# Performance work log

Measured on AMD Instinct MI355X. Metric: run time of the kernel, lower is better.

## Reference

```python
import jax, jax.numpy as jnp
import numpy as np

DIM = 256   # model dim (forced by gate Linear(32,4): d = 32 = DIM//H)
H = 8       # heads (hard-coded by mask.repeat(1,8,1,1))
D = DIM // H
B = 256     # batch
NS = 100    # skeleton tokens (sub-block size)
NQ = 64     # query tokens
N = NS + NQ # 164
NE = 4      # experts
HID = 50    # expert hidden
LN_EPS = 1e-5


def setup_inputs() -> dict:
    key = jax.random.key(0)
    ks = jax.random.split(key, 12)
    s = 0.02
    return {
        "x": jax.random.normal(ks[0], (B, N, DIM), jnp.float32),
        "mask": jax.random.randint(ks[1], (B, N), 0, 2).astype(bool),
        "w_qk_s": jax.random.normal(ks[2], (DIM, 2 * DIM), jnp.float32) * s,
        "w_qk_q": jax.random.normal(ks[3], (DIM, 2 * DIM), jnp.float32) * s,
        "w_v": jax.random.normal(ks[4], (DIM, DIM), jnp.float32) * s,
        "w_gate": jax.random.normal(ks[5], (D, NE), jnp.float32) * s,
        "b_gate": jnp.zeros((NE,), jnp.float32),
        "ln_gamma": jnp.ones((NE,), jnp.float32),
        "ln_beta": jnp.zeros((NE,), jnp.float32),
        "w1": jax.random.normal(ks[6], (NE, NS, HID), jnp.float32) * s,
        "b1": jnp.zeros((NE, HID), jnp.float32),
        "w2": jax.random.normal(ks[7], (NE, HID, NS), jnp.float32) * s,
        "b2": jnp.zeros((NE, NS), jnp.float32),
        "w_out": jax.random.normal(ks[8], (DIM, DIM), jnp.float32) * s,
        "b_out": jnp.zeros((DIM,), jnp.float32),
    }


def reference(x, mask, w_qk_s, w_qk_q, w_v, w_gate, b_gate, ln_gamma, ln_beta,
              w1, b1, w2, b2, w_out, b_out):
    b, n, dim = x.shape
    scale = dim ** -0.5  # scale_with_head=False -> dim**-0.5

    def to_heads(t):  # (b, m, H*D) -> (b, H, m, D)
        return t.reshape(b, -1, H, D).transpose(0, 2, 1, 3)

    # separate qk projections for skeleton (first 100) vs query (last 64) tokens
    q_s, k_s = jnp.split(x[:, :NS] @ w_qk_s, 2, axis=-1)
    q_q, k_q = jnp.split(x[:, NS:] @ w_qk_q, 2, axis=-1)
    q = jnp.concatenate([to_heads(q_s), to_heads(q_q)], axis=2)  # (b,H,N,D)
    k = jnp.concatenate([to_heads(k_s), to_heads(k_q)], axis=2)
    v = to_heads(x @ w_v)

    # gates: RAW reshape of x (b,n,H*D) -> (b,H,n,D) (memory reinterpretation,
    # as in torch x.reshape), detached, sliced to first 100 'rows'
    gx = jax.lax.stop_gradient(x).reshape(b, H, n, D)[:, :, :NS, :]
    g = gx @ w_gate + b_gate                              # (b,H,100,4)
    mu = g.mean(-1, keepdims=True)
    var = g.var(-1, keepdims=True)
    g = (g - mu) / jnp.sqrt(var + LN_EPS) * ln_gamma + ln_beta
    gates = jax.nn.softmax(g, axis=-1)                    # (b,H,100,4)

    dots = jnp.einsum('bhid,bhjd->bhij', q, k) * scale    # (b,H,N,N)
    mask_value = -jnp.finfo(dots.dtype).max
    dots = jnp.where(mask[:, None, None, :], mask_value, dots)

    # soft-MoE over the 100x100 sub-block (experts applied along key axis)
    attn_q = dots[:, :, :NS, :NS]                         # (b,H,100,100)
    h1 = jax.nn.relu(jnp.einsum('bhij,ejk->bheik', jax.nn.relu(attn_q), w1)
                     + b1[:, None, :])                    # (b,H,4,100,50)
    eo = jax.nn.relu(jnp.einsum('bheik,ekj->bheij', h1, w2)
                     + b2[:, None, :])                    # (b,H,4,100,100)
    moes = jnp.einsum('bheij,bhie->bhij', eo, gates)      # (b,H,100,100)

    dots = dots.at[:, :, :NS, :NS].add(moes)
    attn = jax.nn.softmax(dots, axis=-1)
    out = jnp.einsum('bhij,bhjd->bhid', attn, v)          # (b,H,N,D)
    out = out.transpose(0, 2, 1, 3).reshape(b, n, dim)
    return out @ w_out + b_out
```

## Files before the change

kernel.cpp:

```cpp
#include <hip/hip_runtime.h>

typedef __bf16 bf16x8 __attribute__((ext_vector_type(8)));
typedef __bf16 bf16x4 __attribute__((ext_vector_type(4)));
typedef float  f32x4  __attribute__((ext_vector_type(4)));

__device__ __forceinline__ bf16x8 ldb8(const __bf16* p) {
    return *reinterpret_cast<const bf16x8*>(p);
}
__device__ __forceinline__ bf16x8 zero8() {
    bf16x8 z;
    #pragma unroll
    for (int i = 0; i < 8; i++) z[i] = (__bf16)0.f;
    return z;
}
__device__ __forceinline__ __bf16 ldw(const void* p, int i, int m) {
    return m ? (__bf16)((const float*)p)[i] : ((const __bf16*)p)[i];
}
__device__ __forceinline__ bf16x8 ldx8(const void* p, size_t ei, int m) {
    if (m) {
        const float* f = (const float*)p + ei;
        f32x4 a = *reinterpret_cast<const f32x4*>(f);
        f32x4 b = *reinterpret_cast<const f32x4*>(f + 4);
        bf16x8 r;
        #pragma unroll
        for (int u = 0; u < 4; u++) { r[u] = (__bf16)a[u]; r[4 + u] = (__bf16)b[u]; }
        return r;
    }
    return ldb8((const __bf16*)p + ei);
}

__global__ __launch_bounds__(256) void prep_kernel(
    const void* x, const void* mask,
    const void* wqks, const void* wqkq, const void* wv, const void* w1,
    const void* w2, const void* wout, const void* wg, const void* bg,
    const void* lng, const void* lnb, const void* b1, const void* b2,
    const void* bout, int* modes, unsigned* maskb,
    __bf16* __restrict__ Wts, __bf16* __restrict__ Wtq,
    __bf16* __restrict__ w1t, __bf16* __restrict__ w2t,
    __bf16* __restrict__ wot, __bf16* __restrict__ wsm)
{
    __shared__ int sbad;
    const int t = threadIdx.x, bid = blockIdx.x;
    if (t == 0) sbad = 0;
    __syncthreads();
    {
        const unsigned int* xw = (const unsigned int*)x;
        int bad = 0;
        for (int i = t; i < 2048; i += 256) {
            unsigned int w = xw[i];
            unsigned int el = (w >> 7) & 0xFF, eh = (w >> 23) & 0xFF;
            if (el >= 0x94 || el == 0xFF) bad++;
            if (eh >= 0x94 || eh == 0xFF) bad++;
        }
        if (bad) atomicAdd(&sbad, bad);
    }
    __syncthreads();
    const int m = (sbad > 64) ? 1 : 0;

    if (bid >= 1268) {
        __shared__ int v32bad, v16bad;
        __shared__ unsigned mb[24];
        const int mbid = bid - 1268;
        if (t == 0) { v32bad = 0; v16bad = 0; }
        if (t < 24) mb[t] = ((t % 6) == 5) ? 0xFFFFFFF0u : 0u;
        __syncthreads();
        const unsigned int* mw = (const unsigned int*)mask;
        int b32 = 0, b16 = 0;
        for (int i = t; i < 10496; i += 256) {
            unsigned int w = mw[i];
            if (!(w == 0u || w == 1u || w == 0x3F800000u)) b32++;
            unsigned int h0 = w & 0xFFFFu, h1 = w >> 16;
            if (!(h0 == 0u || h0 == 1u || h0 == 0x3F80u)) b16++;
            if (!(h1 == 0u || h1 == 1u || h1 == 0x3F80u)) b16++;
        }
        if (b32) atomicAdd(&v32bad, b32);
        if (b16) atomicAdd(&v16bad, b16);
        __syncthreads();
        const int mmode = (v32bad == 0) ? 0 : ((v16bad == 0) ? 2 : 1);
        if (mbid == 0 && t == 0) { modes[0] = m; modes[1] = mmode; }
        const int lo = mbid * 656;
        for (int i2 = t; i2 < 656; i2 += 256) {
            int i = lo + i2;
            int val;
            if (mmode == 0)      val = (((const int*)mask)[i] != 0);
            else if (mmode == 2) val = (((const unsigned short*)mask)[i] != 0);
            else                 val = (((const unsigned char*)mask)[i] != 0);
            if (val) {
                int ib = i2 / 164, jb = i2 - ib * 164;
                atomicOr(&mb[ib * 6 + (jb >> 5)], 1u << (jb & 31));
            }
        }
        __syncthreads();
        if (t < 24) maskb[mbid * 24 + t] = mb[t];
        return;
    }

    int i = bid * 256 + t;
    if (i < 196608) {
        int n = i >> 8, k = i & 255;
        __bf16 vs, vq;
        if (n < 512) { vs = ldw(wqks, k * 512 + n, m); vq = ldw(wqkq, k * 512 + n, m); }
        else         { vs = ldw(wv, k * 256 + (n - 512), m); vq = vs; }
        Wts[i] = vs; Wtq[i] = vq;
        return;
    }
    i -= 196608;
    if (i < 32768) {
        int e = i >> 13, r = i & 8191, n = r >> 7, k = r & 127;
        __bf16 v = (__bf16)0.f;
        if (n < 50) {
            if (k < 100)       v = ldw(w1, (e * 100 + k) * 50 + n, m);
            else if (k == 100) v = ldw(b1, e * 50 + n, m);
        }
        w1t[i] = v;
        return;
    }
    i -= 32768;
    if (i < 28672) {
        int e = i / 7168, r = i % 7168, n = r >> 6, k = r & 63;
        __bf16 v = (__bf16)0.f;
        if (n < 100) {
            if (k < 50)       v = ldw(w2, (e * 50 + k) * 100 + n, m);
            else if (k == 50) v = ldw(b2, e * 100 + n, m);
        }
        w2t[i] = v;
        return;
    }
    i -= 28672;
    if (i < 65536) {
        int n = i >> 8, k = i & 255;
        wot[i] = ldw(wout, k * 256 + n, m);
        return;
    }
    i -= 65536;
    if (i < 996) {
        __bf16 v;
        if (i < 128)      v = ldw(wg, i, m);
        else if (i < 132) v = ldw(bg, i - 128, m);
        else if (i < 136) v = ldw(lng, i - 132, m);
        else if (i < 140) v = ldw(lnb, i - 136, m);
        else if (i < 340) v = ldw(b1, i - 140, m);
        else if (i < 740) v = ldw(b2, i - 340, m);
        else              v = ldw(bout, i - 740, m);
        wsm[i] = v;
    }
}

__global__ __launch_bounds__(256, 2) void qkv_kernel(
    const void* __restrict__ x, const __bf16* __restrict__ Wts,
    const __bf16* __restrict__ Wtq, const __bf16* __restrict__ wsm,
    const int* __restrict__ modes,
    __bf16* __restrict__ q, __bf16* __restrict__ k, __bf16* __restrict__ vt,
    float* __restrict__ gates)
{
    __shared__ __bf16 xs[32][264];
    __shared__ float wgf[128];
    __shared__ float gcst[12];
    const int m = modes[0];
    const int b = blockIdx.y;
    const int mt = blockIdx.x >> 1;
    const int half = blockIdx.x & 1;
    const __bf16* Wt = (mt < 4) ? Wts : Wtq;
    const int rbase = (mt < 4) ? mt * 32 : 100 + (mt - 4) * 32;
    const int tid = threadIdx.x;

    if (tid < 128) wgf[tid] = (float)wsm[tid];
    if (tid < 12)  gcst[tid] = (float)wsm[128 + tid];
    for (int c = tid; c < 1024; c += 256) {
        int row = c >> 5, part = c & 31;
        bf16x8 val = ldx8(x, ((size_t)b * 164 + rbase + row) * 256 + part * 8, m);
        *reinterpret_cast<bf16x8*>(&xs[row][part * 8]) = val;
    }
    __syncthreads();

    if (half == 0) {
        int jg = rbase * 8 + tid;
        int h = jg / 164;
        int j = jg - h * 164;
        if (j < 100) {
            const __bf16* xp = &xs[tid >> 3][(tid & 7) * 32];
            float g[4] = {gcst[0], gcst[1], gcst[2], gcst[3]};
            #pragma unroll
            for (int p = 0; p < 4; p++) {
                bf16x8 xv = ldb8(xp + p * 8);
                #pragma unroll
                for (int u = 0; u < 8; u++) {
                    float f = (float)xv[u];
                    #pragma unroll
                    for (int e = 0; e < 4; e++) g[e] += f * wgf[(p * 8 + u) * 4 + e];
                }
            }
            float mu = 0.25f * (g[0] + g[1] + g[2] + g[3]);
            float var = 0.25f * ((g[0]-mu)*(g[0]-mu) + (g[1]-mu)*(g[1]-mu) +
                                 (g[2]-mu)*(g[2]-mu) + (g[3]-mu)*(g[3]-mu));
            float is = rsqrtf(var + 1e-5f);
            float mx = -3.0e38f;
            #pragma unroll
            for (int e = 0; e < 4; e++) {
                g[e] = (g[e] - mu) * is * gcst[4 + e] + gcst[8 + e];
                mx = fmaxf(mx, g[e]);
            }
            float s = 0.f;
            #pragma unroll
            for (int e = 0; e < 4; e++) { g[e] = __expf(g[e] - mx); s += g[e]; }
            float inv = 1.f / s;
            float4 gv = make_float4(g[0]*inv, g[1]*inv, g[2]*inv, g[3]*inv);
            *reinterpret_cast<float4*>(&gates[((size_t)(b * 8 + h) * 100 + j) * 4]) = gv;
        }
    }

    const int w = tid >> 6, l = tid & 63, lr = l & 15, lc = l >> 4;
    f32x4 acc[2][6];
    #pragma unroll
    for (int ms = 0; ms < 2; ms++)
        #pragma unroll
        for (int nt = 0; nt < 6; nt++) acc[ms][nt] = (f32x4){0.f, 0.f, 0.f, 0.f};

    #pragma unroll
    for (int kt = 0; kt < 8; kt++) {
        bf16x8 a0 = ldb8(&xs[lr][kt * 32 + lc * 8]);
        bf16x8 a1 = ldb8(&xs[16 + lr][kt * 32 + lc * 8]);
        #pragma unroll
        for (int nt = 0; nt < 6; nt++) {
            bf16x8 bb = ldb8(Wt + (size_t)(half * 384 + w * 96 + nt * 16 + lr) * 256 + kt * 32 + lc * 8);
            acc[0][nt] = __builtin_amdgcn_mfma_f32_16x16x32_bf16(a0, bb, acc[0][nt], 0, 0, 0);
            acc[1][nt] = __builtin_amdgcn_mfma_f32_16x16x32_bf16(a1, bb, acc[1][nt], 0, 0, 0);
        }
    }
    #pragma unroll
    for (int ms = 0; ms < 2; ms++) {
        #pragma unroll
        for (int nt = 0; nt < 6; nt++) {
            int c = half * 384 + w * 96 + nt * 16 + lr;
            int i0 = rbase + ms * 16 + lc * 4;
            if (c < 512) {
                __bf16* dst; int ch;
                if (c < 256) { dst = q; ch = c; }
                else         { dst = k; ch = c - 256; }
                int hh = ch >> 5, d = ch & 31;
                #pragma unroll
                for (int r = 0; r < 4; r++) {
                    int i = i0 + r;
                    if (mt >= 4 || i < 100)
                        dst[(((size_t)b * 8 + hh) * 164 + i) * 32 + d] = (__bf16)acc[ms][nt][r];
                }
            } else {
                int ch = c - 512, hh = ch >> 5, d = ch & 31;
                if (mt >= 4 || i0 < 100) {
                    bf16x4 pv;
                    #pragma unroll
                    for (int r = 0; r < 4; r++) pv[r] = (__bf16)acc[ms][nt][r];
                    *reinterpret_cast<bf16x4*>(&vt[((size_t)(b * 8 + hh) * 32 + d) * 176 + i0]) = pv;
                }
            }
        }
    }
}

__global__ __launch_bounds__(256, 4) void attn_kernel(
    const __bf16* __restrict__ qg, const __bf16* __restrict__ kg,
    const __bf16* __restrict__ vtg, const float* __restrict__ gatesg,
    const unsigned* __restrict__ maskbg, const __bf16* __restrict__ w1t,
    const __bf16* __restrict__ w2t, __bf16* __restrict__ ohg)
{
    __shared__ __align__(16) __bf16 lds[20352];
    const int RS_OFF = 7040;
    const int P_OFF  = 7040;
    const int H1_OFF = 15744;

    const int flat = blockIdx.x;
    const int xcd = flat & 7, j5 = flat >> 3;
    const int bh = ((j5 & 255) << 3) | xcd;
    const int rt = j5 >> 8;
    const int b = bh >> 3, tid = threadIdx.x;
    const int w = tid >> 6, l = tid & 63, lr = l & 15, lc = l >> 4;
    const int m0 = w * 16;
    const bool moe_wave = (rt * 64 + m0) < 100;

    const __bf16* kbase = kg + (size_t)bh * 164 * 32;
    for (int c = tid; c < 656; c += 256) {
        int row = c >> 2, part = c & 3;
        bf16x8 val = ldb8(kbase + row * 32 + part * 8);
        *reinterpret_cast<bf16x8*>(&lds[row * 40 + part * 8]) = val;
    }
    const unsigned* mbp = maskbg + b * 6;
    unsigned mbits = 0;
    #pragma unroll
    for (int nt = 0; nt < 11; nt++)
        mbits |= ((mbp[nt >> 1] >> (((nt & 1) << 4) + lr)) & 1u) << nt;
    int qrow = rt * 64 + m0 + lr; if (qrow > 163) qrow = 163;
    bf16x8 afq = ldb8(qg + ((size_t)bh * 164 + qrow) * 32 + lc * 8);
    __syncthreads();

    f32x4 raw[11];
    __builtin_amdgcn_s_setprio(1);
    #pragma unroll
    for (int nt = 0; nt < 11; nt++) {
        bf16x8 bf = ldb8(&lds[(nt * 16 + lr) * 40 + lc * 8]);
        f32x4 acc = {0.f, 0.f, 0.f, 0.f};
        acc = __builtin_amdgcn_mfma_f32_16x16x32_bf16(afq, bf, acc, 0, 0, 0);
        bool bad = (mbits >> nt) & 1;
        #pragma unroll
        for (int r = 0; r < 4; r++)
            raw[nt][r] = bad ? -1e30f : acc[r] * 0.0625f;
    }
    __builtin_amdgcn_s_setprio(0);

    if (moe_wave) {
        #pragma unroll
        for (int nt = 0; nt < 8; nt++) {
            int j = nt * 16 + lr;
            #pragma unroll
            for (int r = 0; r < 4; r++) {
                float v = raw[nt][r];
                v = (v < 0.f) ? 0.f : v;
                if (j >= 100) v = (j == 100) ? 1.f : 0.f;
                lds[RS_OFF + (m0 + lc * 4 + r) * 136 + j] = (__bf16)v;
            }
        }
    }
    __syncthreads();

    const __bf16* vtb = vtg + (size_t)bh * 32 * 176;
    #pragma unroll
    for (int p = 0; p < 3; p++) {
        int c = tid + p * 256;
        int row = c / 24, jc = c - row * 24, j0 = jc * 8;
        bf16x8 vv;
        if (j0 < 164) {
            vv = ldb8(vtb + row * 176 + j0);
            if (j0 == 160) { vv[4] = (__bf16)0.f; vv[5] = (__bf16)0.f; vv[6] = (__bf16)0.f; vv[7] = (__bf16)0.f; }
        } else vv = zero8();
        *reinterpret_cast<bf16x8*>(&lds[row * 200 + j0]) = vv;
    }

    if (moe_wave) {
        const int gi0 = rt * 64 + m0 + lc * 4;
        for (int e = 0; e < 4; e++) {
            bf16x8 sa[4];
            #pragma unroll
            for (int kt = 0; kt < 4; kt++)
                sa[kt] = ldb8(&lds[RS_OFF + (m0 + lr) * 136 + kt * 32 + lc * 8]);
            #pragma unroll
            for (int nt = 0; nt < 4; nt++) {
                f32x4 acc = {0.f, 0.f, 0.f, 0.f};
                __builtin_amdgcn_s_setprio(1);
                #pragma unroll
                for (int kt = 0; kt < 4; kt++) {
                    bf16x8 bb = ldb8(w1t + (size_t)(e * 64 + nt * 16 + lr) * 128 + kt * 32 + lc * 8);
                    acc = __builtin_amdgcn_mfma_f32_16x16x32_bf16(sa[kt], bb, acc, 0, 0, 0);
                }
                __builtin_amdgcn_s_setprio(0);
                int n = nt * 16 + lr;
                #pragma unroll
                for (int r = 0; r < 4; r++) {
                    float v = acc[r];
                    if (v < 0.f) v = 0.f;
                    if (n == 50) v = 1.f;
                    lds[H1_OFF + (m0 + lc * 4 + r) * 72 + n] = (__bf16)v;
                }
            }
            bf16x8 ha0 = ldb8(&lds[H1_OFF + (m0 + lr) * 72 + lc * 8]);
            bf16x8 ha1 = ldb8(&lds[H1_OFF + (m0 + lr) * 72 + 32 + lc * 8]);
            float gt[4];
            #pragma unroll
            for (int r = 0; r < 4; r++) {
                int gi = gi0 + r;
                gt[r] = (gi < 100) ? gatesg[((size_t)bh * 100 + gi) * 4 + e] : 0.f;
            }
            #pragma unroll
            for (int nt = 0; nt < 7; nt++) {
                f32x4 acc = {0.f, 0.f, 0.f, 0.f};
                __builtin_amdgcn_s_setprio(1);
                bf16x8 bb0 = ldb8(w2t + (size_t)(e * 112 + nt * 16 + lr) * 64 + lc * 8);
                acc = __builtin_amdgcn_mfma_f32_16x16x32_bf16(ha0, bb0, acc, 0, 0, 0);
                bf16x8 bb1 = ldb8(w2t + (size_t)(e * 112 + nt * 16 + lr) * 64 + 32 + lc * 8);
                acc = __builtin_amdgcn_mfma_f32_16x16x32_bf16(ha1, bb1, acc, 0, 0, 0);
                __builtin_amdgcn_s_setprio(0);
                #pragma unroll
                for (int r = 0; r < 4; r++) {
                    float v = acc[r];
                    if (v < 0.f) v = 0.f;
                    raw[nt][r] += v * gt[r];
                }
            }
        }
    }
    __syncthreads();

    #pragma unroll
    for (int r = 0; r < 4; r++) {
        float m2 = raw[0][r];
        #pragma unroll
        for (int nt = 1; nt < 11; nt++) m2 = fmaxf(m2, raw[nt][r]);
        m2 = fmaxf(m2, __shfl_xor(m2, 1, 64));
        m2 = fmaxf(m2, __shfl_xor(m2, 2, 64));
        m2 = fmaxf(m2, __shfl_xor(m2, 4, 64));
        m2 = fmaxf(m2, __shfl_xor(m2, 8, 64));
        float s2 = 0.f;
        #pragma unroll
        for (int nt = 0; nt < 11; nt++) {
            float ev = __expf(raw[nt][r] - m2);
            raw[nt][r] = ev;
            s2 += ev;
        }
        s2 += __shfl_xor(s2, 1, 64);
        s2 += __shfl_xor(s2, 2, 64);
        s2 += __shfl_xor(s2, 4, 64);
        s2 += __shfl_xor(s2, 8, 64);
        float inv = (s2 > 0.f) ? 1.f / s2 : 0.f;
        #pragma unroll
        for (int nt = 0; nt < 11; nt++)
            lds[P_OFF + (m0 + lc * 4 + r) * 200 + nt * 16 + lr] = (__bf16)(raw[nt][r] * inv);
        lds[P_OFF + (m0 + lc * 4 + r) * 200 + 176 + lr] = (__bf16)0.f;
    }
    __syncthreads();

    int gi = rt * 64 + m0 + lr;
    #pragma unroll
    for (int nt = 0; nt < 2; nt++) {
        f32x4 acc = {0.f, 0.f, 0.f, 0.f};
        __builtin_amdgcn_s_setprio(1);
        #pragma unroll
        for (int kt = 0; kt < 6; kt++) {
            bf16x8 va = ldb8(&lds[(nt * 16 + lr) * 200 + kt * 32 + lc * 8]);
            bf16x8 pb = ldb8(&lds[P_OFF + (m0 + lr) * 200 + kt * 32 + lc * 8]);
            acc = __builtin_amdgcn_mfma_f32_16x16x32_bf16(va, pb, acc, 0, 0, 0);
        }
        __builtin_amdgcn_s_setprio(0);
        if (gi < 164) {
            bf16x4 ov;
            #pragma unroll
            for (int r = 0; r < 4; r++) ov[r] = (__bf16)acc[r];
            *reinterpret_cast<bf16x4*>(&ohg[((size_t)bh * 164 + gi) * 32 + nt * 16 + lc * 4]) = ov;
        }
    }
}

__global__ __launch_bounds__(256) void outproj_kernel(
    const __bf16* __restrict__ oh, const __bf16* __restrict__ wot,
    const __bf16* __restrict__ wsm, float* __restrict__ out)
{
    const __bf16* bout = wsm + 740;
    const int b = blockIdx.y;
    const int mt = blockIdx.x >> 2;
    const int ntile = blockIdx.x & 3;
    const int tid = threadIdx.x;
    const int w = tid >> 6, l = tid & 63, lr = l & 15, lc = l >> 4;
    int row = mt * 64 + w * 16 + lr; if (row > 163) row = 163;
    f32x4 acc[4];
    #pragma unroll
    for (int nt = 0; nt < 4; nt++) acc[nt] = (f32x4){0.f, 0.f, 0.f, 0.f};
    #pragma unroll
    for (int kt = 0; kt < 8; kt++) {
        bf16x8 a = ldb8(oh + (((size_t)b * 8 + kt) * 164 + row) * 32 + lc * 8);
        #pragma unroll
        for (int nt = 0; nt < 4; nt++) {
            bf16x8 bb = ldb8(wot + (size_t)(ntile * 64 + nt * 16 + lr) * 256 + kt * 32 + lc * 8);
            acc[nt] = __builtin_amdgcn_mfma_f32_16x16x32_bf16(a, bb, acc[nt], 0, 0, 0);
        }
    }
    #pragma unroll
    for (int nt = 0; nt < 4; nt++) {
        int n = ntile * 64 + nt * 16 + lr;
        float bias = (float)bout[n];
        #pragma unroll
        for (int r = 0; r < 4; r++) {
            int i = mt * 64 + w * 16 + lc * 4 + r;
            if (i < 164)
                out[((size_t)b * 164 + i) * 256 + n] = acc[nt][r] + bias;
        }
    }
}

extern "C" void kernel_launch(void* const* d_in, const int* in_sizes, int n_in,
                              void* d_out, int out_size, void* d_ws, size_t ws_size,
                              hipStream_t stream) {
    const void* x      = d_in[0];
    const void* mask   = d_in[1];
    const void* w_qk_s = d_in[2];
    const void* w_qk_q = d_in[3];
    const void* w_v    = d_in[4];
    const void* w_gate = d_in[5];
    const void* b_gate = d_in[6];
    const void* ln_g   = d_in[7];
    const void* ln_b   = d_in[8];
    const void* w1     = d_in[9];
    const void* b1     = d_in[10];
    const void* w2     = d_in[11];
    const void* b2     = d_in[12];
    const void* w_out  = d_in[13];
    const void* b_out  = d_in[14];
    float* out = (float*)d_out;

    char* ws = (char*)d_ws;
    size_t off = 0;
    auto nextp = [&](size_t bytes) {
        char* p = ws + off;
        off += (bytes + 255) & ~(size_t)255;
        return p;
    };
    const size_t QKV_ELEMS = (size_t)256 * 8 * 164 * 32;
    const size_t VT_ELEMS  = (size_t)256 * 8 * 32 * 176;
    int*      modes  = (int*)nextp(64);
    unsigned* maskb  = (unsigned*)nextp((size_t)256 * 6 * 4);
    __bf16* qws  = (__bf16*)nextp(QKV_ELEMS * 2);
    __bf16* kws  = (__bf16*)nextp(QKV_ELEMS * 2);
    __bf16* vtws = (__bf16*)nextp(VT_ELEMS * 2);
    __bf16* ohws = (__bf16*)nextp(QKV_ELEMS * 2);
    float*  gws  = (float*)nextp((size_t)2048 * 100 * 4 * 4);
    __bf16* Wts  = (__bf16*)nextp(768 * 256 * 2);
    __bf16* Wtq  = (__bf16*)nextp(768 * 256 * 2);
    __bf16* w1t  = (__bf16*)nextp(4 * 64 * 128 * 2);
    __bf16* w2t  = (__bf16*)nextp(4 * 112 * 64 * 2);
    __bf16* wot  = (__bf16*)nextp(256 * 256 * 2);
    __bf16* wsm  = (__bf16*)nextp(996 * 2);

    prep_kernel<<<1332, 256, 0, stream>>>(x, mask, w_qk_s, w_qk_q, w_v, w1, w2,
                                          w_out, w_gate, b_gate, ln_g, ln_b, b1,
                                          b2, b_out, modes, maskb,
                                          Wts, Wtq, w1t, w2t, wot, wsm);
    qkv_kernel<<<dim3(12, 256), 256, 0, stream>>>(x, Wts, Wtq, wsm, modes,
                                                  qws, kws, vtws, gws);
    attn_kernel<<<6144, 256, 0, stream>>>(qws, kws, vtws, gws, maskb,
                                          w1t, w2t, ohws);
    outproj_kernel<<<dim3(12, 256), 256, 0, stream>>>(ohws, wot, wsm, out);
}
```

Before: 490.4 us.

## Give each wave a private LDS region and read K straight from global

Each wave now gets its own LDS scratch slice for the relu'd scores, the MoE hidden tile and the softmax probabilities. This removes the block-wide barriers between the score, MoE and softmax phases, leaving one barrier before the P·V product. K fragments are loaded directly from global memory per wave instead of being staged through shared memory. The V tile load is issued early into registers and written to LDS later to overlap its latency. The cost is more redundant global K reads across waves and higher register pressure from holding the V vectors.

Result: no change. 484.5 us (-1.2%).

```diff
diff --git a/kernel.cpp b/kernel.cpp
--- a/kernel.cpp
+++ b/kernel.cpp
@@ -263,11 +263,7 @@
     const unsigned* __restrict__ maskbg, const __bf16* __restrict__ w1t,
     const __bf16* __restrict__ w2t, __bf16* __restrict__ ohg)
 {
-    __shared__ __align__(16) __bf16 lds[20352];
-    const int RS_OFF = 7040;
-    const int P_OFF  = 7040;
-    const int H1_OFF = 15744;
-
+    __shared__ __align__(16) __bf16 lds[19712];
     const int flat = blockIdx.x;
     const int xcd = flat & 7, j5 = flat >> 3;
     const int bh = ((j5 & 255) << 3) | xcd;
@@ -275,14 +271,37 @@
     const int b = bh >> 3, tid = threadIdx.x;
     const int w = tid >> 6, l = tid & 63, lr = l & 15, lc = l >> 4;
     const int m0 = w * 16;
+    const int WB  = 6400 + w * 3328;
+    const int H1B = WB + 2176;
     const bool moe_wave = (rt * 64 + m0) < 100;
 
-    const __bf16* kbase = kg + (size_t)bh * 164 * 32;
-    for (int c = tid; c < 656; c += 256) {
-        int row = c >> 2, part = c & 3;
-        bf16x8 val = ldb8(kbase + row * 32 + part * 8);
-        *reinterpret_cast<bf16x8*>(&lds[row * 40 + part * 8]) = val;
-    }
+    const __bf16* vtb = vtg + (size_t)bh * 32 * 176;
+    bf16x8 vv0, vv1, vv2;
+    {
+        int c = tid;
+        int row = c / 24, j0 = (c - row * 24) * 8;
+        if (j0 < 164) {
+            vv0 = ldb8(vtb + row * 176 + j0);
+            if (j0 == 160) { vv0[4] = (__bf16)0.f; vv0[5] = (__bf16)0.f; vv0[6] = (__bf16)0.f; vv0[7] = (__bf16)0.f; }
+        } else vv0 = zero8();
+    }
+    {
+        int c = tid + 256;
+        int row = c / 24, j0 = (c - row * 24) * 8;
+        if (j0 < 164) {
+            vv1 = ldb8(vtb + row * 176 + j0);
+            if (j0 == 160) { vv1[4] = (__bf16)0.f; vv1[5] = (__bf16)0.f; vv1[6] = (__bf16)0.f; vv1[7] = (__bf16)0.f; }
+        } else vv1 = zero8();
+    }
+    {
+        int c = tid + 512;
+        int row = c / 24, j0 = (c - row * 24) * 8;
+        if (j0 < 164) {
+            vv2 = ldb8(vtb + row * 176 + j0);
+            if (j0 == 160) { vv2[4] = (__bf16)0.f; vv2[5] = (__bf16)0.f; vv2[6] = (__bf16)0.f; vv2[7] = (__bf16)0.f; }
+        } else vv2 = zero8();
+    }
+
     const unsigned* mbp = maskbg + b * 6;
     unsigned mbits = 0;
     #pragma unroll
@@ -290,21 +309,32 @@
         mbits |= ((mbp[nt >> 1] >> (((nt & 1) << 4) + lr)) & 1u) << nt;
     int qrow = rt * 64 + m0 + lr; if (qrow > 163) qrow = 163;
     bf16x8 afq = ldb8(qg + ((size_t)bh * 164 + qrow) * 32 + lc * 8);
-    __syncthreads();
-
+
+    const __bf16* kbase = kg + (size_t)bh * 164 * 32;
     f32x4 raw[11];
-    __builtin_amdgcn_s_setprio(1);
     #pragma unroll
     for (int nt = 0; nt < 11; nt++) {
-        bf16x8 bf = ldb8(&lds[(nt * 16 + lr) * 40 + lc * 8]);
+        int krow = nt * 16 + lr; if (krow > 163) krow = 163;
+        bf16x8 kb = ldb8(kbase + (size_t)krow * 32 + lc * 8);
         f32x4 acc = {0.f, 0.f, 0.f, 0.f};
-        acc = __builtin_amdgcn_mfma_f32_16x16x32_bf16(afq, bf, acc, 0, 0, 0);
+        acc = __builtin_amdgcn_mfma_f32_16x16x32_bf16(afq, kb, acc, 0, 0, 0);
         bool bad = (mbits >> nt) & 1;
         #pragma unroll
         for (int r = 0; r < 4; r++)
             raw[nt][r] = bad ? -1e30f : acc[r] * 0.0625f;
     }
-    __builtin_amdgcn_s_setprio(0);
+
+    {
+        int c = tid;
+        int row = c / 24, j0 = (c - row * 24) * 8;
+        *reinterpret_cast<bf16x8*>(&lds[row * 200 + j0]) = vv0;
+        c = tid + 256;
+        row = c / 24; j0 = (c - row * 24) * 8;
+        *reinterpret_cast<bf16x8*>(&lds[row * 200 + j0]) = vv1;
+        c = tid + 512;
+        row = c / 24; j0 = (c - row * 24) * 8;
+        *reinterpret_cast<bf16x8*>(&lds[row * 200 + j0]) = vv2;
+    }
 
     if (moe_wave) {
         #pragma unroll
@@ -315,23 +345,9 @@
                 float v = raw[nt][r];
                 v = (v < 0.f) ? 0.f : v;
                 if (j >= 100) v = (j == 100) ? 1.f : 0.f;
-                lds[RS_OFF + (m0 + lc * 4 + r) * 136 + j] = (__bf16)v;
-            }
-        }
-    }
-    __syncthreads();
-
-    const __bf16* vtb = vtg + (size_t)bh * 32 * 176;
-    #pragma unroll
-    for (int p = 0; p < 3; p++) {
-        int c = tid + p * 256;
-        int row = c / 24, jc = c - row * 24, j0 = jc * 8;
-        bf16x8 vv;
-        if (j0 < 164) {
-            vv = ldb8(vtb + row * 176 + j0);
-            if (j0 == 160) { vv[4] = (__bf16)0.f; vv[5] = (__bf16)0.f; vv[6] = (__bf16)0.f; vv[7] = (__bf16)0.f; }
-        } else vv = zero8();
-        *reinterpret_cast<bf16x8*>(&lds[row * 200 + j0]) = vv;
+                lds[WB + (lc * 4 + r) * 136 + j] = (__bf16)v;
+            }
+        }
     }
 
     if (moe_wave) {
@@ -340,7 +356,7 @@
             bf16x8 sa[4];
             #pragma unroll
             for (int kt = 0; kt < 4; kt++)
-                sa[kt] = ldb8(&lds[RS_OFF + (m0 + lr) * 136 + kt * 32 + lc * 8]);
+                sa[kt] = ldb8(&lds[WB + lr * 136 + kt * 32 + lc * 8]);
             #pragma unroll
             for (int nt = 0; nt < 4; nt++) {
                 f32x4 acc = {0.f, 0.f, 0.f, 0.f};
@@ -357,11 +373,11 @@
                     float v = acc[r];
                     if (v < 0.f) v = 0.f;
                     if (n == 50) v = 1.f;
-                    lds[H1_OFF + (m0 + lc * 4 + r) * 72 + n] = (__bf16)v;
+                    lds[H1B + (lc * 4 + r) * 72 + n] = (__bf16)v;
                 }
             }
-            bf16x8 ha0 = ldb8(&lds[H1_OFF + (m0 + lr) * 72 + lc * 8]);
-            bf16x8 ha1 = ldb8(&lds[H1_OFF + (m0 + lr) * 72 + 32 + lc * 8]);
+            bf16x8 ha0 = ldb8(&lds[H1B + lr * 72 + lc * 8]);
+            bf16x8 ha1 = ldb8(&lds[H1B + lr * 72 + 32 + lc * 8]);
             float gt[4];
             #pragma unroll
             for (int r = 0; r < 4; r++) {
@@ -386,7 +402,6 @@
             }
         }
     }
-    __syncthreads();
 
     #pragma unroll
     for (int r = 0; r < 4; r++) {
@@ -411,8 +426,8 @@
         float inv = (s2 > 0.f) ? 1.f / s2 : 0.f;
         #pragma unroll
         for (int nt = 0; nt < 11; nt++)
-            lds[P_OFF + (m0 + lc * 4 + r) * 200 + nt * 16 + lr] = (__bf16)(raw[nt][r] * inv);
-        lds[P_OFF + (m0 + lc * 4 + r) * 200 + 176 + lr] = (__bf16)0.f;
+            lds[WB + (lc * 4 + r) * 200 + nt * 16 + lr] = (__bf16)(raw[nt][r] * inv);
+        lds[WB + (lc * 4 + r) * 200 + 176 + lr] = (__bf16)0.f;
     }
     __syncthreads();
 
@@ -424,7 +439,7 @@
         #pragma unroll
         for (int kt = 0; kt < 6; kt++) {
             bf16x8 va = ldb8(&lds[(nt * 16 + lr) * 200 + kt * 32 + lc * 8]);
-            bf16x8 pb = ldb8(&lds[P_OFF + (m0 + lr) * 200 + kt * 32 + lc * 8]);
+            bf16x8 pb = ldb8(&lds[WB + lr * 200 + kt * 32 + lc * 8]);
             acc = __builtin_amdgcn_mfma_f32_16x16x32_bf16(va, pb, acc, 0, 0, 0);
         }
         __builtin_amdgcn_s_setprio(0);
```
